# Performance work log

Hardware: AMD Instinct MI355X
Metric: run time of the kernel (lower is better)

Reference implementation:

```python
import jax, jax.numpy as jnp
import numpy as np

DIM = 256
N_EMBED = 4096


def setup_inputs() -> dict:
    key = jax.random.key(0)
    k1, k2 = jax.random.split(key)
    input = jax.random.normal(k1, (8, 64, 64, DIM), dtype=jnp.float32)
    embed = jax.random.normal(k2, (DIM, N_EMBED), dtype=jnp.float32)
    return {"input": input, "embed": embed}


def reference(input, embed):
    # flatten: [N, dim]
    flatten = input.reshape(-1, DIM)
    # squared-euclidean distance to each code: [N, n_embed]
    dist = (
        jnp.sum(flatten * flatten, axis=1, keepdims=True)
        - 2.0 * flatten @ embed
        + jnp.sum(embed * embed, axis=0, keepdims=True)
    )
    embed_ind_flat = jnp.argmax(-dist, axis=1)  # nearest code per vector
    embed_ind = embed_ind_flat.reshape(input.shape[:-1])
    # gather codes: embed is [dim, n_embed], codebook rows are embed.T
    quantize = jnp.take(embed.T, embed_ind, axis=0)  # [B, m, n, dim]
    # commitment loss (quantize detached)
    diff = jnp.mean((jax.lax.stop_gradient(quantize) - input) ** 2)
    # straight-through estimator
    quantize = input + jax.lax.stop_gradient(quantize - input)
    return (quantize, diff, embed_ind)
```

## Files before the change

### kernel.cpp

```cpp
#include <hip/hip_runtime.h>
#include <hip/hip_bf16.h>


#define M_ROWS 32768
#define K_DIM 256
#define N_CODES 4096

#define BM 128
#define BN 128
#define BK 32
#define TM 8
#define TN 8

__global__ void norms_kernel(const float* __restrict__ E, float* __restrict__ norms) {
    int j = blockIdx.x * blockDim.x + threadIdx.x;
    if (j >= N_CODES) return;
    float s = 0.f;
    for (int d = 0; d < K_DIM; ++d) {
        float v = E[(size_t)d * N_CODES + j];
        s = fmaf(v, v, s);
    }
    norms[j] = s;
}

__global__ __launch_bounds__(256, 2) void gemm_argmin_kernel(
    const float* __restrict__ F,
    const float* __restrict__ E,
    const float* __restrict__ norms,
    unsigned long long* __restrict__ keys)
{
    __shared__ float As[BK][BM + 4];
    __shared__ float Bs[BK][BN + 4];

    const int bx = blockIdx.x & 31;
    const int by = blockIdx.x >> 5;
    const int bm0 = by * BM;
    const int bn0 = bx * BN;
    const int tid = threadIdx.x;
    const int tx = tid & 15;
    const int ty = tid >> 4;

    float acc[TM][TN];
#pragma unroll
    for (int i = 0; i < TM; ++i)
#pragma unroll
        for (int j = 0; j < TN; ++j) acc[i][j] = 0.f;

    for (int kc = 0; kc < K_DIM; kc += BK) {
        float4 a_reg[4], b_reg[4];
#pragma unroll
        for (int i = 0; i < 4; ++i) {
            int idx = tid + i * 256;
            int m  = idx >> 3, k4 = idx & 7;
            a_reg[i] = *(const float4*)&F[(size_t)(bm0 + m) * K_DIM + kc + k4 * 4];
            int kk = idx >> 5, n4 = idx & 31;
            b_reg[i] = *(const float4*)&E[(size_t)(kc + kk) * N_CODES + bn0 + n4 * 4];
        }
        __syncthreads();
#pragma unroll
        for (int i = 0; i < 4; ++i) {
            int idx = tid + i * 256;
            int m  = idx >> 3, k4 = idx & 7;
            As[k4 * 4 + 0][m] = a_reg[i].x;
            As[k4 * 4 + 1][m] = a_reg[i].y;
            As[k4 * 4 + 2][m] = a_reg[i].z;
            As[k4 * 4 + 3][m] = a_reg[i].w;
            int kk = idx >> 5, n4 = idx & 31;
            *(float4*)&Bs[kk][n4 * 4] = b_reg[i];
        }
        __syncthreads();

#pragma unroll
        for (int k = 0; k < BK; ++k) {
            float a[TM], b[TN];
            *(float4*)&a[0] = *(const float4*)&As[k][ty * TM];
            *(float4*)&a[4] = *(const float4*)&As[k][ty * TM + 4];
            *(float4*)&b[0] = *(const float4*)&Bs[k][tx * TN];
            *(float4*)&b[4] = *(const float4*)&Bs[k][tx * TN + 4];
#pragma unroll
            for (int i = 0; i < TM; ++i)
#pragma unroll
                for (int j = 0; j < TN; ++j)
                    acc[i][j] = fmaf(a[i], b[j], acc[i][j]);
        }
    }

    float nrm[TN];
#pragma unroll
    for (int j = 0; j < TN; ++j) nrm[j] = norms[bn0 + tx * TN + j];

#pragma unroll
    for (int i = 0; i < TM; ++i) {
        float best = INFINITY;
        int bestj = 0;
#pragma unroll
        for (int j = 0; j < TN; ++j) {
            float d = fmaf(-2.f, acc[i][j], nrm[j]);
            if (d < best) { best = d; bestj = bn0 + tx * TN + j; }
        }
        unsigned u = __float_as_uint(best);
        u = (u & 0x80000000u) ? ~u : (u | 0x80000000u);
        unsigned long long key = ((unsigned long long)u << 32) | (unsigned)bestj;
#pragma unroll
        for (int s = 1; s < 16; s <<= 1) {
            unsigned long long o = __shfl_xor(key, s, 64);
            if (o < key) key = o;
        }
        if (tx == 0) atomicMin(&keys[bm0 + ty * TM + i], key);
    }
}

__global__ void gather_kernel(
    const float* __restrict__ F,
    const float* __restrict__ E,
    const unsigned long long* __restrict__ keys,
    float* __restrict__ q_out,
    float* __restrict__ diff_out,
    float* __restrict__ ind_out)
{
    const int lane = threadIdx.x & 63;
    const int wave = (blockIdx.x * (blockDim.x >> 6)) + (threadIdx.x >> 6);
    const int nwaves = gridDim.x * (blockDim.x >> 6);

    float dsum = 0.f;
    for (int row = wave; row < M_ROWS; row += nwaves) {
        unsigned long long key = keys[row];
        int ind = (int)(key & 0xFFFFFFFFull);
        if (lane == 0) ind_out[row] = (float)ind;
#pragma unroll
        for (int t = 0; t < 4; ++t) {
            int d = lane + t * 64;
            float x = F[(size_t)row * K_DIM + d];
            float q = E[(size_t)d * N_CODES + ind];
            float delta = q - x;
            q_out[(size_t)row * K_DIM + d] = x + delta;
            dsum = fmaf(delta, delta, dsum);
        }
    }
#pragma unroll
    for (int s = 32; s >= 1; s >>= 1) dsum += __shfl_xor(dsum, s, 64);
    if (lane == 0)
        atomicAdd(diff_out, dsum * (1.0f / ((float)M_ROWS * (float)K_DIM)));
}

extern "C" void kernel_launch(void* const* d_in, const int* in_sizes, int n_in,
                              void* d_out, int out_size, void* d_ws, size_t ws_size,
                              hipStream_t stream) {
    const float* F = (const float*)d_in[0];
    const float* E = (const float*)d_in[1];

    float* q_out    = (float*)d_out;
    float* diff_out = (float*)d_out + (size_t)M_ROWS * K_DIM;
    float* ind_out  = diff_out + 1;

    float* norms = (float*)d_ws;
    unsigned long long* keys = (unsigned long long*)((char*)d_ws + 16384);

    hipMemsetAsync(keys, 0xFF, (size_t)M_ROWS * 8, stream);
    hipMemsetAsync(diff_out, 0, 4, stream);

    norms_kernel<<<N_CODES / 256, 256, 0, stream>>>(E, norms);
    gemm_argmin_kernel<<<(M_ROWS / BM) * (N_CODES / BN), 256, 0, stream>>>(F, E, norms, keys);
    gather_kernel<<<1024, 256, 0, stream>>>(F, E, keys, q_out, diff_out, ind_out);
}
```

Baseline: 985.8 us.

## Use bf16 MFMA screening pass with exact fp32 rescoring of near-best candidates

```diff
diff --git a/kernel.cpp b/kernel.cpp
--- a/kernel.cpp
+++ b/kernel.cpp
@@ -6,11 +6,236 @@
 #define K_DIM 256
 #define N_CODES 4096
 
-#define BM 128
-#define BN 128
-#define BK 32
-#define TM 8
-#define TN 8
+typedef __attribute__((ext_vector_type(8))) short short8v;
+typedef __attribute__((ext_vector_type(4))) float f32x4;
+
+__device__ inline unsigned long long packKey(float d, int idx) {
+    unsigned u = __float_as_uint(d);
+    u = (u & 0x80000000u) ? ~u : (u | 0x80000000u);
+    return ((unsigned long long)u << 32) | (unsigned)idx;
+}
+__device__ inline float unpackDist(unsigned long long k) {
+    unsigned u = (unsigned)(k >> 32);
+    u = (u & 0x80000000u) ? (u & 0x7FFFFFFFu) : ~u;
+    return __uint_as_float(u);
+}
+__device__ inline unsigned short f2bf(float x) {
+    __hip_bfloat16 h = __float2bfloat16(x);
+    return *reinterpret_cast<unsigned short*>(&h);
+}
+
+__global__ void transpose_kernel(const float* __restrict__ E,
+                                 float* __restrict__ Et,
+                                 unsigned short* __restrict__ Ethi) {
+    __shared__ float tile[64][65];
+    const int kb = blockIdx.x & 3;
+    const int jb = blockIdx.x >> 2;
+    const int t = threadIdx.x;
+#pragma unroll
+    for (int it = 0; it < 16; ++it) {
+        int linear = it * 256 + t;
+        int kk = linear >> 6, jj = linear & 63;
+        tile[kk][jj] = E[(size_t)(kb * 64 + kk) * N_CODES + jb * 64 + jj];
+    }
+    __syncthreads();
+#pragma unroll
+    for (int it = 0; it < 16; ++it) {
+        int linear = it * 256 + t;
+        int jj = linear >> 6, kk = linear & 63;
+        float v = tile[kk][jj];
+        size_t o = (size_t)(jb * 64 + jj) * K_DIM + kb * 64 + kk;
+        Et[o] = v;
+        Ethi[o] = f2bf(v);
+    }
+}
+
+__global__ void nrm_et_kernel(const float* __restrict__ Et,
+                              float* __restrict__ nrm,
+                              float* __restrict__ maxnrm) {
+    const int l = threadIdx.x & 63;
+    const int j = blockIdx.x * 4 + (threadIdx.x >> 6);
+    float4 v = *(const float4*)&Et[(size_t)j * K_DIM + l * 4];
+    float s = v.x * v.x;
+    s = fmaf(v.y, v.y, s); s = fmaf(v.z, v.z, s); s = fmaf(v.w, v.w, s);
+#pragma unroll
+    for (int sh = 32; sh >= 1; sh >>= 1) s += __shfl_xor(s, sh, 64);
+    if (l == 0) {
+        nrm[j] = s;
+        atomicMax((int*)maxnrm, __float_as_int(s));
+    }
+}
+
+__global__ void splitF_kernel(const float* __restrict__ F,
+                              unsigned short* __restrict__ Fhi,
+                              float* __restrict__ thrAdd,
+                              const float* __restrict__ maxnrm) {
+    const int l = threadIdx.x & 63;
+    const int row = blockIdx.x * 4 + (threadIdx.x >> 6);
+    float4 v = *(const float4*)&F[(size_t)row * K_DIM + l * 4];
+    ushort4 h;
+    h.x = f2bf(v.x); h.y = f2bf(v.y); h.z = f2bf(v.z); h.w = f2bf(v.w);
+    *(ushort4*)&Fhi[(size_t)row * K_DIM + l * 4] = h;
+    float s = v.x * v.x;
+    s = fmaf(v.y, v.y, s); s = fmaf(v.z, v.z, s); s = fmaf(v.w, v.w, s);
+#pragma unroll
+    for (int sh = 32; sh >= 1; sh >>= 1) s += __shfl_xor(s, sh, 64);
+    if (l == 0) {
+        thrAdd[row] = 0.0314f * sqrtf(s) * sqrtf(maxnrm[0]) + 0.05f;
+    }
+}
+
+template<int PASS>
+__global__ __launch_bounds__(256, 2) void gemm_bf16_kernel(
+    const unsigned short* __restrict__ Fhi,
+    const unsigned short* __restrict__ Ethi,
+    const float* __restrict__ nrm,
+    const float* __restrict__ thrAdd,
+    const unsigned long long* __restrict__ keysIn,
+    unsigned long long* __restrict__ keysOut,
+    const float* __restrict__ Fx,
+    const float* __restrict__ Et)
+{
+    __shared__ unsigned short sA[128 * 64];
+    __shared__ unsigned short sB[128 * 64];
+    const int tid = threadIdx.x;
+    const int l = tid & 63;
+    const int wid = tid >> 6;
+    const int bx = blockIdx.x & 31, by = blockIdx.x >> 5;
+    const int bm0 = by * 128, bn0 = bx * 128;
+    const int wm = wid >> 1, wn = wid & 1;
+
+    f32x4 acc[4][4];
+#pragma unroll
+    for (int mi = 0; mi < 4; ++mi)
+#pragma unroll
+        for (int ni = 0; ni < 4; ++ni) acc[mi][ni] = (f32x4){0.f, 0.f, 0.f, 0.f};
+
+    const int srow = l >> 3;
+    const int kch = (l & 7) ^ srow;
+
+    for (int kt = 0; kt < 4; ++kt) {
+        const int k0 = kt * 64;
+#pragma unroll
+        for (int i = 0; i < 4; ++i) {
+            const int q = wid * 4 + i;
+            const int rowA = q * 8 + srow;
+            __builtin_amdgcn_global_load_lds(
+                (const __attribute__((address_space(1))) unsigned int*)
+                    (Fhi + (size_t)(bm0 + rowA) * K_DIM + k0 + kch * 8),
+                (__attribute__((address_space(3))) unsigned int*)(&sA[q * 512]),
+                16, 0, 0);
+            __builtin_amdgcn_global_load_lds(
+                (const __attribute__((address_space(1))) unsigned int*)
+                    (Ethi + (size_t)(bn0 + rowA) * K_DIM + k0 + kch * 8),
+                (__attribute__((address_space(3))) unsigned int*)(&sB[q * 512]),
+                16, 0, 0);
+        }
+        __syncthreads();
+
+#pragma unroll
+        for (int s = 0; s < 2; ++s) {
+            short8v af[4], bfv[4];
+#pragma unroll
+            for (int mi = 0; mi < 4; ++mi) {
+                int row = wm * 64 + mi * 16 + (l & 15);
+                int ch = (s * 4 + (l >> 4)) ^ (l & 7);
+                af[mi] = *(const short8v*)&sA[row * 64 + ch * 8];
+            }
+#pragma unroll
+            for (int ni = 0; ni < 4; ++ni) {
+                int col = wn * 64 + ni * 16 + (l & 15);
+                int ch = (s * 4 + (l >> 4)) ^ (l & 7);
+                bfv[ni] = *(const short8v*)&sB[col * 64 + ch * 8];
+            }
+#pragma unroll
+            for (int mi = 0; mi < 4; ++mi)
+#pragma unroll
+                for (int ni = 0; ni < 4; ++ni)
+                    acc[mi][ni] = __builtin_amdgcn_mfma_f32_16x16x32_bf16(
+                        af[mi], bfv[ni], acc[mi][ni], 0, 0, 0);
+        }
+        __syncthreads();
+    }
+
+    float nrmv[4];
+#pragma unroll
+    for (int ni = 0; ni < 4; ++ni)
+        nrmv[ni] = nrm[bn0 + wn * 64 + ni * 16 + (l & 15)];
+
+    if (PASS == 1) {
+#pragma unroll
+        for (int mi = 0; mi < 4; ++mi)
+#pragma unroll
+            for (int rr = 0; rr < 4; ++rr) {
+                int rg = bm0 + wm * 64 + mi * 16 + (l >> 4) * 4 + rr;
+                float best = INFINITY; int bc = 0;
+#pragma unroll
+                for (int ni = 0; ni < 4; ++ni) {
+                    float d = fmaf(-2.f, acc[mi][ni][rr], nrmv[ni]);
+                    if (d < best) { best = d; bc = bn0 + wn * 64 + ni * 16 + (l & 15); }
+                }
+                unsigned long long key = packKey(best, bc);
+#pragma unroll
+                for (int sh = 1; sh < 16; sh <<= 1) {
+                    unsigned long long o = __shfl_xor(key, sh, 64);
+                    if (o < key) key = o;
+                }
+                if ((l & 15) == 0) atomicMin(&keysOut[rg], key);
+            }
+    } else {
+#pragma unroll
+        for (int mi = 0; mi < 4; ++mi)
+#pragma unroll
+            for (int rr = 0; rr < 4; ++rr) {
+                int rg = bm0 + wm * 64 + mi * 16 + (l >> 4) * 4 + rr;
+                float thr = unpackDist(keysIn[rg]) + thrAdd[rg];
+#pragma unroll
+                for (int ni = 0; ni < 4; ++ni) {
+                    float d = fmaf(-2.f, acc[mi][ni][rr], nrmv[ni]);
+                    if (d <= thr) {
+                        int c = bn0 + wn * 64 + ni * 16 + (l & 15);
+                        const float4* fr = (const float4*)(Fx + (size_t)rg * K_DIM);
+                        const float4* er = (const float4*)(Et + (size_t)c * K_DIM);
+                        float ex = 0.f;
+                        for (int k4 = 0; k4 < 64; ++k4) {
+                            float4 a = fr[k4], b = er[k4];
+                            ex = fmaf(a.x, b.x, ex); ex = fmaf(a.y, b.y, ex);
+                            ex = fmaf(a.z, b.z, ex); ex = fmaf(a.w, b.w, ex);
+                        }
+                        float dex = fmaf(-2.f, ex, nrmv[ni]);
+                        atomicMin(&keysOut[rg], packKey(dex, c));
+                    }
+                }
+            }
+    }
+}
+
+__global__ void gather_kernel(const float* __restrict__ F,
+                              const float* __restrict__ Et,
+                              const unsigned long long* __restrict__ keys,
+                              float* __restrict__ q_out,
+                              float* __restrict__ diff_out,
+                              float* __restrict__ ind_out) {
+    const int l = threadIdx.x & 63;
+    const int wave = blockIdx.x * 4 + (threadIdx.x >> 6);
+    const int nw = gridDim.x * 4;
+    float dsum = 0.f;
+    for (int row = wave; row < M_ROWS; row += nw) {
+        int ind = (int)(keys[row] & 0xFFFFFFFFull);
+        if (l == 0) ind_out[row] = (float)ind;
+        float4 x = *(const float4*)&F[(size_t)row * K_DIM + l * 4];
+        float4 e = *(const float4*)&Et[(size_t)ind * K_DIM + l * 4];
+        float dx = e.x - x.x, dy = e.y - x.y, dz = e.z - x.z, dw = e.w - x.w;
+        float4 o = {x.x + dx, x.y + dy, x.z + dz, x.w + dw};
+        *(float4*)&q_out[(size_t)row * K_DIM + l * 4] = o;
+        dsum = fmaf(dx, dx, dsum); dsum = fmaf(dy, dy, dsum);
+        dsum = fmaf(dz, dz, dsum); dsum = fmaf(dw, dw, dsum);
+    }
+#pragma unroll
+    for (int sh = 32; sh >= 1; sh >>= 1) dsum += __shfl_xor(dsum, sh, 64);
+    if (l == 0)
+        atomicAdd(diff_out, dsum * (1.0f / ((float)M_ROWS * (float)K_DIM)));
+}
 
 __global__ void norms_kernel(const float* __restrict__ E, float* __restrict__ norms) {
     int j = blockIdx.x * blockDim.x + threadIdx.x;
@@ -24,34 +249,25 @@
 }
 
 __global__ __launch_bounds__(256, 2) void gemm_argmin_kernel(
-    const float* __restrict__ F,
-    const float* __restrict__ E,
-    const float* __restrict__ norms,
-    unsigned long long* __restrict__ keys)
-{
-    __shared__ float As[BK][BM + 4];
-    __shared__ float Bs[BK][BN + 4];
-
-    const int bx = blockIdx.x & 31;
-    const int by = blockIdx.x >> 5;
-    const int bm0 = by * BM;
-    const int bn0 = bx * BN;
+    const float* __restrict__ F, const float* __restrict__ E,
+    const float* __restrict__ norms, unsigned long long* __restrict__ keys) {
+    __shared__ float As[32][132];
+    __shared__ float Bs[32][132];
+    const int bx = blockIdx.x & 31, by = blockIdx.x >> 5;
+    const int bm0 = by * 128, bn0 = bx * 128;
     const int tid = threadIdx.x;
-    const int tx = tid & 15;
-    const int ty = tid >> 4;
-
-    float acc[TM][TN];
-#pragma unroll
-    for (int i = 0; i < TM; ++i)
-#pragma unroll
-        for (int j = 0; j < TN; ++j) acc[i][j] = 0.f;
-
-    for (int kc = 0; kc < K_DIM; kc += BK) {
+    const int tx = tid & 15, ty = tid >> 4;
+    float acc[8][8];
+#pragma unroll
+    for (int i = 0; i < 8; ++i)
+#pragma unroll
+        for (int j = 0; j < 8; ++j) acc[i][j] = 0.f;
+    for (int kc = 0; kc < K_DIM; kc += 32) {
         float4 a_reg[4], b_reg[4];
 #pragma unroll
         for (int i = 0; i < 4; ++i) {
             int idx = tid + i * 256;
-            int m  = idx >> 3, k4 = idx & 7;
+            int m = idx >> 3, k4 = idx & 7;
             a_reg[i] = *(const float4*)&F[(size_t)(bm0 + m) * K_DIM + kc + k4 * 4];
             int kk = idx >> 5, n4 = idx & 31;
             b_reg[i] = *(const float4*)&E[(size_t)(kc + kk) * N_CODES + bn0 + n4 * 4];
@@ -60,72 +276,58 @@
 #pragma unroll
         for (int i = 0; i < 4; ++i) {
             int idx = tid + i * 256;
-            int m  = idx >> 3, k4 = idx & 7;
-            As[k4 * 4 + 0][m] = a_reg[i].x;
-            As[k4 * 4 + 1][m] = a_reg[i].y;
-            As[k4 * 4 + 2][m] = a_reg[i].z;
-            As[k4 * 4 + 3][m] = a_reg[i].w;
+            int m = idx >> 3, k4 = idx & 7;
+            As[k4 * 4 + 0][m] = a_reg[i].x; As[k4 * 4 + 1][m] = a_reg[i].y;
+            As[k4 * 4 + 2][m] = a_reg[i].z; As[k4 * 4 + 3][m] = a_reg[i].w;
             int kk = idx >> 5, n4 = idx & 31;
             *(float4*)&Bs[kk][n4 * 4] = b_reg[i];
         }
         __syncthreads();
-
-#pragma unroll
-        for (int k = 0; k < BK; ++k) {
-            float a[TM], b[TN];
-            *(float4*)&a[0] = *(const float4*)&As[k][ty * TM];
-            *(float4*)&a[4] = *(const float4*)&As[k][ty * TM + 4];
-            *(float4*)&b[0] = *(const float4*)&Bs[k][tx * TN];
-            *(float4*)&b[4] = *(const float4*)&Bs[k][tx * TN + 4];
-#pragma unroll
-            for (int i = 0; i < TM; ++i)
-#pragma unroll
-                for (int j = 0; j < TN; ++j)
-                    acc[i][j] = fmaf(a[i], b[j], acc[i][j]);
-        }
-    }
-
-    float nrm[TN];
-#pragma unroll
-    for (int j = 0; j < TN; ++j) nrm[j] = norms[bn0 + tx * TN + j];
-
-#pragma unroll
-    for (int i = 0; i < TM; ++i) {
-        float best = INFINITY;
-        int bestj = 0;
-#pragma unroll
-        for (int j = 0; j < TN; ++j) {
-            float d = fmaf(-2.f, acc[i][j], nrm[j]);
-            if (d < best) { best = d; bestj = bn0 + tx * TN + j; }
-        }
-        unsigned u = __float_as_uint(best);
-        u = (u & 0x80000000u) ? ~u : (u | 0x80000000u);
-        unsigned long long key = ((unsigned long long)u << 32) | (unsigned)bestj;
+#pragma unroll
+        for (int k = 0; k < 32; ++k) {
+            float a[8], b[8];
+            *(float4*)&a[0] = *(const float4*)&As[k][ty * 8];
+            *(float4*)&a[4] = *(const float4*)&As[k][ty * 8 + 4];
+            *(float4*)&b[0] = *(const float4*)&Bs[k][tx * 8];
+            *(float4*)&b[4] = *(const float4*)&Bs[k][tx * 8 + 4];
+#pragma unroll
+            for (int i = 0; i < 8; ++i)
+#pragma unroll
+                for (int j = 0; j < 8; ++j) acc[i][j] = fmaf(a[i], b[j], acc[i][j]);
+        }
+    }
+    float nrm8[8];
+#pragma unroll
+    for (int j = 0; j < 8; ++j) nrm8[j] = norms[bn0 + tx * 8 + j];
+#pragma unroll
+    for (int i = 0; i < 8; ++i) {
+        float best = INFINITY; int bestj = 0;
+#pragma unroll
+        for (int j = 0; j < 8; ++j) {
+            float d = fmaf(-2.f, acc[i][j], nrm8[j]);
+            if (d < best) { best = d; bestj = bn0 + tx * 8 + j; }
+        }
+        unsigned long long key = packKey(best, bestj);
 #pragma unroll
         for (int s = 1; s < 16; s <<= 1) {
             unsigned long long o = __shfl_xor(key, s, 64);
             if (o < key) key = o;
         }
-        if (tx == 0) atomicMin(&keys[bm0 + ty * TM + i], key);
-    }
-}
-
-__global__ void gather_kernel(
-    const float* __restrict__ F,
-    const float* __restrict__ E,
+        if (tx == 0) atomicMin(&keys[bm0 + ty * 8 + i], key);
+    }
+}
+
+__global__ void gather_legacy_kernel(
+    const float* __restrict__ F, const float* __restrict__ E,
     const unsigned long long* __restrict__ keys,
-    float* __restrict__ q_out,
-    float* __restrict__ diff_out,
-    float* __restrict__ ind_out)
-{
+    float* __restrict__ q_out, float* __restrict__ diff_out,
+    float* __restrict__ ind_out) {
     const int lane = threadIdx.x & 63;
     const int wave = (blockIdx.x * (blockDim.x >> 6)) + (threadIdx.x >> 6);
     const int nwaves = gridDim.x * (blockDim.x >> 6);
-
     float dsum = 0.f;
     for (int row = wave; row < M_ROWS; row += nwaves) {
-        unsigned long long key = keys[row];
-        int ind = (int)(key & 0xFFFFFFFFull);
+        int ind = (int)(keys[row] & 0xFFFFFFFFull);
         if (lane == 0) ind_out[row] = (float)ind;
 #pragma unroll
         for (int t = 0; t < 4; ++t) {
@@ -149,17 +351,49 @@
     const float* F = (const float*)d_in[0];
     const float* E = (const float*)d_in[1];
 
-    float* q_out    = (float*)d_out;
-    float* diff_out = (float*)d_out + (size_t)M_ROWS * K_DIM;
-    float* ind_out  = diff_out + 1;
-
-    float* norms = (float*)d_ws;
-    unsigned long long* keys = (unsigned long long*)((char*)d_ws + 16384);
-
-    hipMemsetAsync(keys, 0xFF, (size_t)M_ROWS * 8, stream);
-    hipMemsetAsync(diff_out, 0, 4, stream);
-
-    norms_kernel<<<N_CODES / 256, 256, 0, stream>>>(E, norms);
-    gemm_argmin_kernel<<<(M_ROWS / BM) * (N_CODES / BN), 256, 0, stream>>>(F, E, norms, keys);
-    gather_kernel<<<1024, 256, 0, stream>>>(F, E, keys, q_out, diff_out, ind_out);
-}
+    float* q_out = (float*)d_out;
+    float* diff_out = q_out + (size_t)M_ROWS * K_DIM;
+    float* ind_out = diff_out + 1;
+
+    const size_t off_nrm = 0;
+    const size_t off_thr = 16384;
+    const size_t off_mx = 147456;
+    const size_t off_k1 = 147712;
+    const size_t off_k2 = 409856;
+    const size_t off_Et = 672768;
+    const size_t off_Ethi = 4867072;
+    const size_t off_Fhi = 6964224;
+    const size_t NEED = 23741440;
+
+    if (ws_size >= NEED) {
+        float* nrm = (float*)((char*)d_ws + off_nrm);
+        float* thrAdd = (float*)((char*)d_ws + off_thr);
+        float* maxnrm = (float*)((char*)d_ws + off_mx);
+        unsigned long long* keysA = (unsigned long long*)((char*)d_ws + off_k1);
+        unsigned long long* keysB = (unsigned long long*)((char*)d_ws + off_k2);
+        float* Et = (float*)((char*)d_ws + off_Et);
+        unsigned short* Ethi = (unsigned short*)((char*)d_ws + off_Ethi);
+        unsigned short* Fhi = (unsigned short*)((char*)d_ws + off_Fhi);
+
+        hipMemsetAsync(keysA, 0xFF, 2 * (size_t)M_ROWS * 8, stream);
+        hipMemsetAsync(maxnrm, 0, 4, stream);
+        hipMemsetAsync(diff_out, 0, 4, stream);
+
+        transpose_kernel<<<256, 256, 0, stream>>>(E, Et, Ethi);
+        nrm_et_kernel<<<1024, 256, 0, stream>>>(Et, nrm, maxnrm);
+        splitF_kernel<<<8192, 256, 0, stream>>>(F, Fhi, thrAdd, maxnrm);
+        gemm_bf16_kernel<1><<<8192, 256, 0, stream>>>(
+            Fhi, Ethi, nrm, thrAdd, keysA, keysA, F, Et);
+        gemm_bf16_kernel<2><<<8192, 256, 0, stream>>>(
+            Fhi, Ethi, nrm, thrAdd, keysA, keysB, F, Et);
+        gather_kernel<<<2048, 256, 0, stream>>>(F, Et, keysB, q_out, diff_out, ind_out);
+    } else {
+        float* norms = (float*)d_ws;
+        unsigned long long* keys = (unsigned long long*)((char*)d_ws + 16384);
+        hipMemsetAsync(keys, 0xFF, (size_t)M_ROWS * 8, stream);
+        hipMemsetAsync(diff_out, 0, 4, stream);
+        norms_kernel<<<N_CODES / 256, 256, 0, stream>>>(E, norms);
+        gemm_argmin_kernel<<<(M_ROWS / 128) * (N_CODES / 128), 256, 0, stream>>>(F, E, norms, keys);
+        gather_legacy_kernel<<<1024, 256, 0, stream>>>(F, E, keys, q_out, diff_out, ind_out);
+    }
+}
```

New measurement: 1.037 ms. 5.2% more time.
